# Kernel tuning notes

Measured on AMD Instinct MI355X. Metric: run time of the kernel, lower is better.

The kernel has to match this reference:

```python
import jax, jax.numpy as jnp
import numpy as np

FILTER = 3
STRIDE = 1


def setup_inputs() -> dict:
    key = jax.random.key(0)
    ks = jax.random.split(key, 6)
    B, P, N, d_in, d_ein, d_model = 16, 4, 4096, 128, 32, 128
    e_dim = FILTER * (FILTER - 1) * d_ein  # 192
    adj = jax.random.uniform(ks[0], (N, N), jnp.float32)
    features = jax.random.normal(ks[1], (B, N, d_in), jnp.float32)
    edge_features = jax.random.normal(ks[2], (B, N, e_dim), jnp.float32)
    mask = jax.random.uniform(ks[3], (P, N, 1), jnp.float32)
    W = jax.random.normal(ks[4], (FILTER * d_in + e_dim, d_model), jnp.float32) * 0.02
    b = jnp.zeros((d_model,), jnp.float32)
    return dict(adj=adj, features=features, edge_features=edge_features, mask=mask, W=W, b=b)


def reference(adj, features, edge_features, mask, W, b):
    Fs, S = FILTER, STRIDE
    B, N, d_in = features.shape
    # padding rule from _padding(): below_pad = filter - (N % stride or stride)
    below_pad = N % S
    below_pad = S if below_pad == 0 else below_pad
    below_pad = Fs - below_pad  # = 2 for stride=1, filter=3
    n_out = (N + below_pad - Fs) // S + 1  # = N

    feat_pad = jnp.pad(features, ((0, 0), (0, below_pad), (0, 0)))
    idx = jnp.arange(n_out)[:, None] * S + jnp.arange(Fs)[None, :]  # [n_out, F]
    win = feat_pad[:, idx, :]  # [B, n_out, F, d_in] (gather = torch unfold windows)
    jump = win.mean(axis=2)    # features.unfold(...).sum(-1)/filter -> [B, n_out, d_in]
    # torch unfold puts filter dim last: [B, n_out, d_in, F]; flatten(-2,-1) is d_in-major
    feat_flat = jnp.swapaxes(win, -1, -2).reshape(B, n_out, Fs * d_in)

    mask_pad = jnp.pad(mask, ((0, 0), (0, below_pad), (0, 0)))
    m = mask_pad[:, idx, :].max(axis=2)  # [P, n_out, 1]

    feat_cat = jnp.concatenate([feat_flat, edge_features], axis=-1)  # [B, n_out, 576]
    out = jax.nn.relu(feat_cat @ W + b)  # dropout is identity in eval
    res = out + jump  # residual (res=True)

    P = m.shape[0]
    d_model = out.shape[-1]
    out_m = (m * out.reshape(-1, P, n_out, d_model)).reshape(-1, n_out, d_model)
    res_m = (m * res.reshape(-1, P, n_out, d_model)).reshape(-1, n_out, d_model)
    return adj, res_m, out_m, m
```

## Files before the change

kernel.cpp:

```cpp
#include <hip/hip_runtime.h>
#include <hip/hip_bf16.h>

typedef __attribute__((ext_vector_type(8))) short short8;
typedef __attribute__((ext_vector_type(4))) float floatx4;

#define NN     4096
#define DIN    128
#define EDIM   192
#define DMODEL 128
#define TM     128
#define LDSP   104

__device__ __forceinline__ unsigned short f2bf(float f) {
    union { float f; unsigned int i; } x; x.f = f;
    unsigned int u = x.i;
    u += 0x7FFFu + ((u >> 16) & 1u);
    return (unsigned short)(u >> 16);
}

__global__ void prep_w(const float* __restrict__ W, unsigned short* __restrict__ wf) {
    const int t = blockIdx.x * 256 + threadIdx.x;
    const int j    = t & 7;
    const int lane = (t >> 3) & 63;
    const int ct   = (t >> 9) & 7;
    const int s    = t >> 12;
    const int k = s * 32 + (lane >> 4) * 8 + j;
    const int n = ct * 16 + (lane & 15);
    wf[t] = f2bf(W[k * DMODEL + n]);
}

__global__ void prep_m(const float* __restrict__ mask,
                       float* __restrict__ m3f, float* __restrict__ o_m) {
    const int t = blockIdx.x * 256 + threadIdx.x;
    const int i = t & (NN - 1);
    float v = mask[t];
    if (i + 1 < NN) v = fmaxf(v, mask[t + 1]);
    if (i + 2 < NN) v = fmaxf(v, mask[t + 2]);
    m3f[t] = v;
    o_m[t] = v;
}

__global__ __launch_bounds__(256) void main_k(
    const float* __restrict__ feat,
    const float* __restrict__ edgef,
    const unsigned short* __restrict__ wfrag,
    const float* __restrict__ bias,
    const float* __restrict__ m3f,
    float* __restrict__ o_res,
    float* __restrict__ o_out)
{
    __shared__ unsigned short Alds[TM * LDSP];

    const int tid  = threadIdx.x;
    const int lane = tid & 63;
    const int wv   = tid >> 6;
    const int nn   = lane & 15;
    const int quad = lane >> 4;

    const int blk = blockIdx.x;
    const int b   = blk >> 5;
    const int i0  = (blk & 31) << 7;

    const float* fb = feat  + (size_t)b * NN * DIN;
    const float* eb = edgef + (size_t)b * NN * EDIM;

    floatx4 acc[2][8];
    #pragma unroll
    for (int rt = 0; rt < 2; ++rt)
        #pragma unroll
        for (int ct = 0; ct < 8; ++ct)
            acc[rt][ct] = (floatx4){0.f, 0.f, 0.f, 0.f};

    for (int ch = 0; ch < 6; ++ch) {
        __syncthreads();
        if (ch < 4) {
            const int c0 = ch << 5;
            const int q4 = tid & 7;
            const int rb = tid >> 3;
            #pragma unroll
            for (int j = 0; j < 3; ++j) {
                #pragma unroll
                for (int it = 0; it < 4; ++it) {
                    const int r   = it * 32 + rb;
                    const int row = i0 + r + j;
                    float4 v = make_float4(0.f, 0.f, 0.f, 0.f);
                    if (row < NN)
                        v = *(const float4*)(fb + (size_t)row * DIN + c0 + q4 * 4);
                    const int la = r * LDSP + q4 * 12 + j;
                    Alds[la]     = f2bf(v.x);
                    Alds[la + 3] = f2bf(v.y);
                    Alds[la + 6] = f2bf(v.z);
                    Alds[la + 9] = f2bf(v.w);
                }
            }
        } else {
            const int e0 = (ch - 4) * 96;
            #pragma unroll
            for (int it = 0; it < 6; ++it) {
                const int q  = it * 256 + tid;
                const int r  = q / 12;
                const int q8 = q - r * 12;
                const float* src = eb + (size_t)(i0 + r) * EDIM + e0 + q8 * 8;
                const float4 v0 = *(const float4*)(src);
                const float4 v1 = *(const float4*)(src + 4);
                short8 s8;
                s8[0] = (short)f2bf(v0.x); s8[1] = (short)f2bf(v0.y);
                s8[2] = (short)f2bf(v0.z); s8[3] = (short)f2bf(v0.w);
                s8[4] = (short)f2bf(v1.x); s8[5] = (short)f2bf(v1.y);
                s8[6] = (short)f2bf(v1.z); s8[7] = (short)f2bf(v1.w);
                *(short8*)(&Alds[r * LDSP + q8 * 8]) = s8;
            }
        }
        __syncthreads();

        #pragma unroll
        for (int s = 0; s < 3; ++s) {
            const int gs = ch * 3 + s;
            short8 bfr[8];
            #pragma unroll
            for (int ct = 0; ct < 8; ++ct)
                bfr[ct] = ((const short8*)wfrag)[(gs * 8 + ct) * 64 + lane];
            short8 afr[2];
            #pragma unroll
            for (int rt = 0; rt < 2; ++rt)
                afr[rt] = *(const short8*)(&Alds[(wv * 32 + rt * 16 + nn) * LDSP + s * 32 + quad * 8]);
            #pragma unroll
            for (int rt = 0; rt < 2; ++rt)
                #pragma unroll
                for (int ct = 0; ct < 8; ++ct)
                    acc[rt][ct] = __builtin_amdgcn_mfma_f32_16x16x32_bf16(
                        afr[rt], bfr[ct], acc[rt][ct], 0, 0, 0);
        }
    }

    float biasv[8];
    #pragma unroll
    for (int ct = 0; ct < 8; ++ct)
        biasv[ct] = bias[ct * 16 + nn];

    const int   p    = b & 3;
    const float inv3 = 1.0f / 3.0f;

    #pragma unroll
    for (int rt = 0; rt < 2; ++rt) {
        const int rbase = wv * 32 + rt * 16 + quad * 4;
        float mv[4];
        #pragma unroll
        for (int reg = 0; reg < 4; ++reg)
            mv[reg] = m3f[p * NN + i0 + rbase + reg];
        #pragma unroll
        for (int ct = 0; ct < 8; ++ct) {
            const int col = ct * 16 + nn;
            float fv[6];
            #pragma unroll
            for (int t6 = 0; t6 < 6; ++t6) {
                const int row = i0 + rbase + t6;
                fv[t6] = (row < NN) ? fb[(size_t)row * DIN + col] : 0.f;
            }
            #pragma unroll
            for (int reg = 0; reg < 4; ++reg) {
                float o = acc[rt][ct][reg] + biasv[ct];
                o = fmaxf(o, 0.f);
                const float jmp = (fv[reg] + fv[reg + 1] + fv[reg + 2]) * inv3;
                const size_t off = ((size_t)b * NN + (i0 + rbase + reg)) * DMODEL + col;
                const float mm = mv[reg];
                o_out[off] = mm * o;
                o_res[off] = mm * (o + jmp);
            }
        }
    }
}

extern "C" void kernel_launch(void* const* d_in, const int* in_sizes, int n_in,
                              void* d_out, int out_size, void* d_ws, size_t ws_size,
                              hipStream_t stream) {
    const float* adj   = (const float*)d_in[0];
    const float* feat  = (const float*)d_in[1];
    const float* edgef = (const float*)d_in[2];
    const float* mask  = (const float*)d_in[3];
    const float* W     = (const float*)d_in[4];
    const float* bias  = (const float*)d_in[5];

    float* out   = (float*)d_out;
    float* o_adj = out;
    float* o_res = out + (size_t)16777216;
    float* o_out = o_res + (size_t)8388608;
    float* o_m   = o_out + (size_t)8388608;

    unsigned short* wfrag = (unsigned short*)d_ws;
    float*          m3f   = (float*)((char*)d_ws + 73728 * 2);

    hipMemcpyAsync(o_adj, adj, (size_t)16777216 * 4, hipMemcpyDeviceToDevice, stream);

    prep_w<<<288, 256, 0, stream>>>(W, wfrag);
    prep_m<<<64, 256, 0, stream>>>(mask, m3f, o_m);
    main_k<<<512, 256, 0, stream>>>(feat, edgef, wfrag, bias, m3f, o_res, o_out);
}
```

Before: 279.8 us.

## Permute W rows to drop LDS staging and load GEMM A-fragments directly

```diff
diff --git a/kernel.cpp b/kernel.cpp
--- a/kernel.cpp
+++ b/kernel.cpp
@@ -8,8 +8,6 @@
 #define DIN    128
 #define EDIM   192
 #define DMODEL 128
-#define TM     128
-#define LDSP   104
 
 __device__ __forceinline__ unsigned short f2bf(float f) {
     union { float f; unsigned int i; } x; x.f = f;
@@ -18,15 +16,31 @@
     return (unsigned short)(u >> 16);
 }
 
+__device__ __forceinline__ unsigned int pk2(float lo, float hi) {
+    union { __hip_bfloat162 v; unsigned int u; } cv;
+    cv.v = __float22bfloat162_rn(make_float2(lo, hi));
+    return cv.u;
+}
+
+__device__ __forceinline__ short8 cvt8(const float4 a, const float4 b) {
+    union { short8 s; unsigned int u[4]; } r;
+    r.u[0] = pk2(a.x, a.y);
+    r.u[1] = pk2(a.z, a.w);
+    r.u[2] = pk2(b.x, b.y);
+    r.u[3] = pk2(b.z, b.w);
+    return r.s;
+}
+
 __global__ void prep_w(const float* __restrict__ W, unsigned short* __restrict__ wf) {
     const int t = blockIdx.x * 256 + threadIdx.x;
-    const int j    = t & 7;
+    const int jj   = t & 7;
     const int lane = (t >> 3) & 63;
     const int ct   = (t >> 9) & 7;
-    const int s    = t >> 12;
-    const int k = s * 32 + (lane >> 4) * 8 + j;
+    const int gs   = t >> 12;
+    const int kt = gs * 32 + ((lane >> 4) << 3) + jj;
+    const int korig = (kt < 384) ? ((kt & 127) * 3 + (kt >> 7)) : kt;
     const int n = ct * 16 + (lane & 15);
-    wf[t] = f2bf(W[k * DMODEL + n]);
+    wf[t] = f2bf(W[korig * DMODEL + n]);
 }
 
 __global__ void prep_m(const float* __restrict__ mask,
@@ -40,7 +54,15 @@
     o_m[t] = v;
 }
 
-__global__ __launch_bounds__(256) void main_k(
+__global__ __launch_bounds__(256) void copy_adj(const float4* __restrict__ src,
+                                                float4* __restrict__ dst) {
+    int idx = blockIdx.x * 256 + threadIdx.x;
+    #pragma unroll
+    for (int i = 0; i < 16; ++i)
+        dst[idx + i * 262144] = src[idx + i * 262144];
+}
+
+__global__ __launch_bounds__(256, 2) void main_k(
     const float* __restrict__ feat,
     const float* __restrict__ edgef,
     const unsigned short* __restrict__ wfrag,
@@ -49,8 +71,6 @@
     float* __restrict__ o_res,
     float* __restrict__ o_out)
 {
-    __shared__ unsigned short Alds[TM * LDSP];
-
     const int tid  = threadIdx.x;
     const int lane = tid & 63;
     const int wv   = tid >> 6;
@@ -64,6 +84,8 @@
     const float* fb = feat  + (size_t)b * NN * DIN;
     const float* eb = edgef + (size_t)b * NN * EDIM;
 
+    const int rowb = i0 + wv * 32 + nn;
+
     floatx4 acc[2][8];
     #pragma unroll
     for (int rt = 0; rt < 2; ++rt)
@@ -71,59 +93,30 @@
         for (int ct = 0; ct < 8; ++ct)
             acc[rt][ct] = (floatx4){0.f, 0.f, 0.f, 0.f};
 
-    for (int ch = 0; ch < 6; ++ch) {
-        __syncthreads();
-        if (ch < 4) {
-            const int c0 = ch << 5;
-            const int q4 = tid & 7;
-            const int rb = tid >> 3;
-            #pragma unroll
-            for (int j = 0; j < 3; ++j) {
-                #pragma unroll
-                for (int it = 0; it < 4; ++it) {
-                    const int r   = it * 32 + rb;
-                    const int row = i0 + r + j;
-                    float4 v = make_float4(0.f, 0.f, 0.f, 0.f);
-                    if (row < NN)
-                        v = *(const float4*)(fb + (size_t)row * DIN + c0 + q4 * 4);
-                    const int la = r * LDSP + q4 * 12 + j;
-                    Alds[la]     = f2bf(v.x);
-                    Alds[la + 3] = f2bf(v.y);
-                    Alds[la + 6] = f2bf(v.z);
-                    Alds[la + 9] = f2bf(v.w);
+    const short8* wf8 = (const short8*)wfrag;
+
+    #pragma unroll
+    for (int j = 0; j < 3; ++j) {
+        #pragma unroll
+        for (int sl = 0; sl < 4; ++sl) {
+            const int gs = j * 4 + sl;
+            short8 bfr[8];
+            #pragma unroll
+            for (int ct = 0; ct < 8; ++ct)
+                bfr[ct] = wf8[(gs * 8 + ct) * 64 + lane];
+            short8 afr[2];
+            #pragma unroll
+            for (int rt = 0; rt < 2; ++rt) {
+                const int row = rowb + rt * 16 + j;
+                float4 a0 = make_float4(0.f, 0.f, 0.f, 0.f);
+                float4 a1 = a0;
+                if (row < NN) {
+                    const float* s = fb + (size_t)row * DIN + sl * 32 + quad * 8;
+                    a0 = *(const float4*)s;
+                    a1 = *(const float4*)(s + 4);
                 }
+                afr[rt] = cvt8(a0, a1);
             }
-        } else {
-            const int e0 = (ch - 4) * 96;
-            #pragma unroll
-            for (int it = 0; it < 6; ++it) {
-                const int q  = it * 256 + tid;
-                const int r  = q / 12;
-                const int q8 = q - r * 12;
-                const float* src = eb + (size_t)(i0 + r) * EDIM + e0 + q8 * 8;
-                const float4 v0 = *(const float4*)(src);
-                const float4 v1 = *(const float4*)(src + 4);
-                short8 s8;
-                s8[0] = (short)f2bf(v0.x); s8[1] = (short)f2bf(v0.y);
-                s8[2] = (short)f2bf(v0.z); s8[3] = (short)f2bf(v0.w);
-                s8[4] = (short)f2bf(v1.x); s8[5] = (short)f2bf(v1.y);
-                s8[6] = (short)f2bf(v1.z); s8[7] = (short)f2bf(v1.w);
-                *(short8*)(&Alds[r * LDSP + q8 * 8]) = s8;
-            }
-        }
-        __syncthreads();
-
-        #pragma unroll
-        for (int s = 0; s < 3; ++s) {
-            const int gs = ch * 3 + s;
-            short8 bfr[8];
-            #pragma unroll
-            for (int ct = 0; ct < 8; ++ct)
-                bfr[ct] = ((const short8*)wfrag)[(gs * 8 + ct) * 64 + lane];
-            short8 afr[2];
-            #pragma unroll
-            for (int rt = 0; rt < 2; ++rt)
-                afr[rt] = *(const short8*)(&Alds[(wv * 32 + rt * 16 + nn) * LDSP + s * 32 + quad * 8]);
             #pragma unroll
             for (int rt = 0; rt < 2; ++rt)
                 #pragma unroll
@@ -131,6 +124,30 @@
                     acc[rt][ct] = __builtin_amdgcn_mfma_f32_16x16x32_bf16(
                         afr[rt], bfr[ct], acc[rt][ct], 0, 0, 0);
         }
+    }
+
+    #pragma unroll
+    for (int eg = 0; eg < 6; ++eg) {
+        const int gs = 12 + eg;
+        short8 bfr[8];
+        #pragma unroll
+        for (int ct = 0; ct < 8; ++ct)
+            bfr[ct] = wf8[(gs * 8 + ct) * 64 + lane];
+        short8 afr[2];
+        #pragma unroll
+        for (int rt = 0; rt < 2; ++rt) {
+            const int row = rowb + rt * 16;
+            const float* s = eb + (size_t)row * EDIM + eg * 32 + quad * 8;
+            const float4 a0 = *(const float4*)s;
+            const float4 a1 = *(const float4*)(s + 4);
+            afr[rt] = cvt8(a0, a1);
+        }
+        #pragma unroll
+        for (int rt = 0; rt < 2; ++rt)
+            #pragma unroll
+            for (int ct = 0; ct < 8; ++ct)
+                acc[rt][ct] = __builtin_amdgcn_mfma_f32_16x16x32_bf16(
+                    afr[rt], bfr[ct], acc[rt][ct], 0, 0, 0);
     }
 
     float biasv[8];
@@ -190,8 +207,7 @@
     unsigned short* wfrag = (unsigned short*)d_ws;
     float*          m3f   = (float*)((char*)d_ws + 73728 * 2);
 
-    hipMemcpyAsync(o_adj, adj, (size_t)16777216 * 4, hipMemcpyDeviceToDevice, stream);
-
+    copy_adj<<<1024, 256, 0, stream>>>((const float4*)adj, (float4*)o_adj);
     prep_w<<<288, 256, 0, stream>>>(W, wfrag);
     prep_m<<<64, 256, 0, stream>>>(mask, m3f, o_m);
     main_k<<<512, 256, 0, stream>>>(feat, edgef, wfrag, bias, m3f, o_res, o_out);
```

After: 284.0 us. No clear change (+1.5%).
